# Kernel optimization log

Measured on AMD Instinct MI355X. Metric: run time of the kernel, lower is better.

## Reference

```python
import jax, jax.numpy as jnp
import numpy as np

D = 1024        # hidden_size = input_size = output_size
E = 8           # num_experts
K = 2           # top-k
TEMP = 1.0      # router temperature


def setup_inputs() -> dict:
    key = jax.random.key(0)
    ks = jax.random.split(key, 7)
    s = 0.02
    x = jax.random.normal(ks[0], (4, 2048, D), dtype=jnp.float32)
    w_router = jax.random.normal(ks[1], (D, E), dtype=jnp.float32) * s
    w1 = jax.random.normal(ks[2], (E, D, D), dtype=jnp.float32) * s
    b1 = jnp.zeros((E, D), dtype=jnp.float32)
    w2 = jax.random.normal(ks[3], (E, D, D), dtype=jnp.float32) * s
    b2 = jnp.zeros((E, D), dtype=jnp.float32)
    return {"x": x, "w_router": w_router, "w1": w1, "b1": b1, "w2": w2, "b2": b2}


def reference(x, w_router, w1, b1, w2, b2):
    B, S, _ = x.shape
    # Router: temperature-scaled logits, softmax, top-k
    logits = jnp.einsum('bsd,de->bse', x, w_router) / TEMP          # [B,S,E]
    probs = jax.nn.softmax(logits, axis=-1)
    top_k_probs, top_k_idx = jax.lax.top_k(probs, K)                # [B,S,K]
    xt = x.reshape(-1, D)                                           # [T,D]
    idx = top_k_idx.reshape(-1, K)                                  # [T,K]
    pk = top_k_probs.reshape(-1, K)                                 # [T,K]
    # Dense expert eval: every expert on every token (faithful to source)
    h = jax.nn.gelu(jnp.einsum('td,edh->eth', xt, w1) + b1[:, None, :])
    expert_out = jnp.einsum('eth,ehd->etd', h, w2) + b2[:, None, :]  # [E,T,D]
    expert_out = jnp.transpose(expert_out, (1, 0, 2))                # [T,E,D]
    # Gather selected experts and combine with routing probs
    sel = jnp.take_along_axis(expert_out, idx[:, :, None], axis=1)   # [T,K,D]
    combined = jnp.sum(sel * pk[:, :, None], axis=1)                 # [T,D]
    return combined.reshape(B, S, D), logits
```

## Files before the change

kernel.cpp:

```cpp
#include <hip/hip_runtime.h>
#include <hip/hip_bf16.h>

#define DH 1024
#define NE 8
#define NT 8192
#define NTK 16384
#define BM 128
#define BN 128
#define BK 64
#define KT (DH / BK)

typedef __bf16 bf16x8 __attribute__((ext_vector_type(8)));
typedef float f32x4 __attribute__((ext_vector_type(4)));
typedef unsigned short u16;
typedef u16 u16x8 __attribute__((ext_vector_type(8)));
typedef u16 u16x4 __attribute__((ext_vector_type(4)));

__device__ __forceinline__ u16 f2bf(float f) {
  union { float f; unsigned u; } v; v.f = f;
  return (u16)((v.u + 0x7fffu + ((v.u >> 16) & 1u)) >> 16);
}
__device__ __forceinline__ float bf2f(u16 h) {
  union { unsigned u; float f; } v; v.u = ((unsigned)h) << 16;
  return v.f;
}
__device__ __forceinline__ float gelu_tanh(float v) {
  float y = 0.7978845608028654f * (v + 0.044715f * v * v * v);
  float t = 1.f - 2.f / (1.f + __expf(2.f * y));
  return 0.5f * v * (1.f + t);
}

__device__ __forceinline__ void gload_lds16(const u16* g, u16* l) {
  __builtin_amdgcn_global_load_lds(
      (const __attribute__((address_space(1))) void*)g,
      (__attribute__((address_space(3))) void*)l, 16, 0, 0);
}

__global__ __launch_bounds__(256) void prep_transpose(
    const float* __restrict__ w1, const float* __restrict__ w2,
    u16* __restrict__ w1t, u16* __restrict__ w2t) {
  __shared__ float tile[64][65];
  int z = blockIdx.z;
  const float* src = (z < NE) ? (w1 + (size_t)z * DH * DH) : (w2 + (size_t)(z - NE) * DH * DH);
  u16* dst = (z < NE) ? (w1t + (size_t)z * DH * DH) : (w2t + (size_t)(z - NE) * DH * DH);
  int d0 = blockIdx.y * 64, n0 = blockIdx.x * 64;
  int tid = threadIdx.x;
  int c = tid & 63, r = tid >> 6;
#pragma unroll
  for (int it = 0; it < 16; ++it) {
    int rr = r + it * 4;
    tile[rr][c] = src[(size_t)(d0 + rr) * DH + n0 + c];
  }
  __syncthreads();
#pragma unroll
  for (int it = 0; it < 16; ++it) {
    int rr = r + it * 4;
    dst[(size_t)(n0 + rr) * DH + d0 + c] = f2bf(tile[c][rr]);
  }
}

__global__ __launch_bounds__(256) void router_kernel(
    const float* __restrict__ x, const float* __restrict__ wr,
    float* __restrict__ logits_out, int* __restrict__ tkidx,
    float* __restrict__ tkp, int* __restrict__ counts,
    u16* __restrict__ xb) {
  __shared__ float wsh[NE][DH + 8];
  __shared__ int hist[NE];
  int tid = threadIdx.x;
  for (int i = tid; i < DH * NE; i += 256) {
    int d = i >> 3, e = i & 7;
    wsh[e][d] = wr[i];
  }
  if (tid < NE) hist[tid] = 0;
  __syncthreads();

  int lane = tid & 63;
  int wv = tid >> 6;
  int t0 = blockIdx.x * 32 + wv * 8;
#pragma unroll 1
  for (int i = 0; i < 8; ++i) {
    int t = t0 + i;
    const float4* xp = (const float4*)(x + (size_t)t * DH);
    u16* xbrow = xb + (size_t)t * DH;
    float a[8] = {0.f, 0.f, 0.f, 0.f, 0.f, 0.f, 0.f, 0.f};
#pragma unroll
    for (int it = 0; it < 4; ++it) {
      float4 xv = xp[it * 64 + lane];
      int d0 = (it * 64 + lane) * 4;
      u16x4 c4;
      c4[0] = f2bf(xv.x); c4[1] = f2bf(xv.y); c4[2] = f2bf(xv.z); c4[3] = f2bf(xv.w);
      *(u16x4*)(xbrow + d0) = c4;
#pragma unroll
      for (int e = 0; e < 8; ++e) {
        float4 w4 = *(const float4*)&wsh[e][d0];
        a[e] += xv.x * w4.x + xv.y * w4.y + xv.z * w4.z + xv.w * w4.w;
      }
    }
#pragma unroll
    for (int off = 32; off; off >>= 1) {
#pragma unroll
      for (int e = 0; e < 8; ++e) a[e] += __shfl_xor(a[e], off, 64);
    }
    if (lane < 8) logits_out[(size_t)t * NE + lane] = a[lane];
    if (lane == 0) {
      float m1 = a[0]; int i1 = 0;
#pragma unroll
      for (int e = 1; e < 8; ++e) if (a[e] > m1) { m1 = a[e]; i1 = e; }
      float m2 = -3.4e38f; int i2 = 0;
#pragma unroll
      for (int e = 0; e < 8; ++e) if (e != i1 && a[e] > m2) { m2 = a[e]; i2 = e; }
      float den = 0.f;
#pragma unroll
      for (int e = 0; e < 8; ++e) den += expf(a[e] - m1);
      tkidx[2 * t] = i1; tkidx[2 * t + 1] = i2;
      tkp[2 * t] = 1.0f / den;
      tkp[2 * t + 1] = expf(m2 - m1) / den;
      atomicAdd(&hist[i1], 1);
      atomicAdd(&hist[i2], 1);
    }
  }
  __syncthreads();
  if (tid < NE) atomicAdd(&counts[tid], hist[tid]);
}

__global__ void offsets_kernel(const int* __restrict__ counts,
                               int* __restrict__ offs, int* __restrict__ cur,
                               int* __restrict__ tmap) {
  if (threadIdx.x == 0) {
    int s = 0;
    for (int e = 0; e < NE; ++e) { offs[e] = s; s += counts[e]; cur[e] = 0; }
    offs[NE] = s;
    int t = 0;
    for (int e = 0; e < NE; ++e)
      for (int m0 = 0; m0 < counts[e]; m0 += BM) {
        tmap[1 + 2 * t] = e; tmap[2 + 2 * t] = m0; ++t;
      }
    tmap[0] = t;
  }
}

__global__ __launch_bounds__(1024) void scatter_kernel(
    const int* __restrict__ tkidx, const float* __restrict__ tkp,
    const int* __restrict__ offs, int* __restrict__ cur,
    int* __restrict__ rows, int* __restrict__ posof, float* __restrict__ pp) {
  __shared__ int h[NE];
  __shared__ int base[NE];
  int tid = threadIdx.x;
  int gid = blockIdx.x * 1024 + tid;
  if (tid < NE) h[tid] = 0;
  __syncthreads();
  int e = tkidx[gid];
  int myrank = atomicAdd(&h[e], 1);
  __syncthreads();
  if (tid < NE) base[tid] = atomicAdd(&cur[tid], h[tid]);
  __syncthreads();
  int pos = offs[e] + base[e] + myrank;
  rows[pos] = gid >> 1;
  posof[gid] = pos;
  pp[pos] = tkp[gid];
}

template <int GELU>
__global__ __launch_bounds__(256, 2) void gemm_kernel(
    const u16* __restrict__ A, const u16* __restrict__ W,
    const float* __restrict__ bias, const int* __restrict__ counts,
    const int* __restrict__ offs, const int* __restrict__ rows,
    const int* __restrict__ tmap, u16* __restrict__ outb) {
  int ty = blockIdx.y;
  if (ty >= tmap[0]) return;
  int e = tmap[1 + 2 * ty];
  int m0 = tmap[2 + 2 * ty];
  int cnt = counts[e];
  int seg = offs[e];
  int n0 = blockIdx.x * BN;

  __shared__ __attribute__((aligned(16))) u16 lds[2][(BM + BN) * BK];

  int tid = threadIdx.x;
  int lane = tid & 63;
  int wv = tid >> 6;

  int srow = tid >> 3;
  int schunk = ((tid & 7) ^ ((tid >> 3) & 7)) * 8;
  const u16* aSrc[4];
  const u16* bSrc[4];
#pragma unroll
  for (int i = 0; i < 4; ++i) {
    int gi = m0 + i * 32 + srow;
    int cl = gi < cnt ? gi : cnt - 1;
    int arow = GELU ? rows[seg + cl] : (seg + cl);
    aSrc[i] = A + (size_t)arow * DH + schunk;
    bSrc[i] = W + (size_t)e * DH * DH + (size_t)(n0 + i * 32 + srow) * DH + schunk;
  }

  auto stage = [&](int d, int k0) {
    u16* base = &lds[d][0];
#pragma unroll
    for (int i = 0; i < 4; ++i) {
      gload_lds16(aSrc[i] + k0, base + (i * 32 + wv * 8) * BK);
      gload_lds16(bSrc[i] + k0, base + BM * BK + (i * 32 + wv * 8) * BK);
    }
  };

  int lr = lane & 15;
  int quad = lane >> 4;
  int sx = lr & 7;
  int k0off = (quad ^ sx) * 8;
  int k1off = ((4 + quad) ^ sx) * 8;
  int wrr = (wv >> 1) * 64, wcc = (wv & 1) * 64;

  f32x4 acc[4][4] = {};

  auto compute = [&](int d) {
    const u16* Ab = &lds[d][0];
    const u16* Bb = &lds[d][BM * BK];
    bf16x8 bfr[2][4];
#pragma unroll
    for (int n = 0; n < 4; ++n) {
      const u16* br = Bb + (size_t)(wcc + n * 16 + lr) * BK;
      bfr[0][n] = *(const bf16x8*)(br + k0off);
      bfr[1][n] = *(const bf16x8*)(br + k1off);
    }
    __builtin_amdgcn_s_setprio(1);
#pragma unroll
    for (int m = 0; m < 4; ++m) {
      const u16* ar = Ab + (size_t)(wrr + m * 16 + lr) * BK;
      bf16x8 a0 = *(const bf16x8*)(ar + k0off);
      bf16x8 a1 = *(const bf16x8*)(ar + k1off);
#pragma unroll
      for (int n = 0; n < 4; ++n) {
        acc[m][n] = __builtin_amdgcn_mfma_f32_16x16x32_bf16(a0, bfr[0][n], acc[m][n], 0, 0, 0);
        acc[m][n] = __builtin_amdgcn_mfma_f32_16x16x32_bf16(a1, bfr[1][n], acc[m][n], 0, 0, 0);
      }
    }
    __builtin_amdgcn_s_setprio(0);
  };

  stage(0, 0);
  stage(1, BK);
#pragma unroll 1
  for (int t = 0; t < KT - 2; ++t) {
    asm volatile("s_waitcnt vmcnt(8)" ::: "memory");
    __builtin_amdgcn_s_barrier();
    asm volatile("" ::: "memory");
    compute(t & 1);
    asm volatile("" ::: "memory");
    __builtin_amdgcn_s_barrier();
    stage(t & 1, (t + 2) * BK);
  }
  asm volatile("s_waitcnt vmcnt(8)" ::: "memory");
  __builtin_amdgcn_s_barrier();
  asm volatile("" ::: "memory");
  compute((KT - 2) & 1);
  asm volatile("s_waitcnt vmcnt(0)" ::: "memory");
  __builtin_amdgcn_s_barrier();
  asm volatile("" ::: "memory");
  compute((KT - 1) & 1);

  int r4 = quad * 4;
  const float* be = bias + (size_t)e * DH;
#pragma unroll
  for (int m = 0; m < 4; ++m) {
#pragma unroll
    for (int n = 0; n < 4; ++n) {
      int col = n0 + wcc + n * 16 + lr;
      float bvv = be[col];
#pragma unroll
      for (int j = 0; j < 4; ++j) {
        int gr = m0 + wrr + m * 16 + r4 + j;
        if (gr < cnt) {
          float v = acc[m][n][j] + bvv;
          if (GELU) v = gelu_tanh(v);
          outb[(size_t)(seg + gr) * DH + col] = f2bf(v);
        }
      }
    }
  }
}

__global__ __launch_bounds__(256) void combine_kernel(
    const u16* __restrict__ eo, const float* __restrict__ tkp,
    const int* __restrict__ posof, float* __restrict__ out) {
  int gid = blockIdx.x * 256 + threadIdx.x;
  int t = gid >> 8;
  int n = (gid & 255) * 4;
  float p0 = tkp[2 * t], p1 = tkp[2 * t + 1];
  int q0 = posof[2 * t], q1 = posof[2 * t + 1];
  u16x4 a = *(const u16x4*)(eo + (size_t)q0 * DH + n);
  u16x4 b = *(const u16x4*)(eo + (size_t)q1 * DH + n);
  float4 o;
  o.x = p0 * bf2f(a[0]) + p1 * bf2f(b[0]);
  o.y = p0 * bf2f(a[1]) + p1 * bf2f(b[1]);
  o.z = p0 * bf2f(a[2]) + p1 * bf2f(b[2]);
  o.w = p0 * bf2f(a[3]) + p1 * bf2f(b[3]);
  *(float4*)(out + (size_t)t * DH + n) = o;
}

extern "C" void kernel_launch(void* const* d_in, const int* in_sizes, int n_in,
                              void* d_out, int out_size, void* d_ws, size_t ws_size,
                              hipStream_t stream) {
  const float* x = (const float*)d_in[0];
  const float* w_router = (const float*)d_in[1];
  const float* w1 = (const float*)d_in[2];
  const float* b1 = (const float*)d_in[3];
  const float* w2 = (const float*)d_in[4];
  const float* b2 = (const float*)d_in[5];
  float* out = (float*)d_out;
  float* logits = out + (size_t)NT * DH;

  char* ws = (char*)d_ws;
  size_t off = 0;
  auto alloc = [&](size_t bytes) -> void* {
    void* p = ws + off;
    off = (off + bytes + 255) & ~(size_t)255;
    return p;
  };
  int* ctrl = (int*)alloc(256);
  int* counts = ctrl;
  int* cur = ctrl + 8;
  int* offs = ctrl + 16;
  int* tmap = (int*)alloc(2048);
  int* tkidx = (int*)alloc((size_t)NTK * 4);
  float* tkp = (float*)alloc((size_t)NTK * 4);
  int* rows = (int*)alloc((size_t)NTK * 4);
  int* posof = (int*)alloc((size_t)NTK * 4);
  float* pp = (float*)alloc((size_t)NTK * 4);
  u16* w1t = (u16*)alloc((size_t)NE * DH * DH * 2);
  u16* w2t = (u16*)alloc((size_t)NE * DH * DH * 2);
  u16* hbuf = (u16*)alloc((size_t)NTK * DH * 2);
  u16* eo = (u16*)alloc((size_t)NTK * DH * 2);
  u16* xb = eo;

  hipMemsetAsync(ctrl, 0, 256, stream);

  prep_transpose<<<dim3(16, 16, 16), 256, 0, stream>>>(w1, w2, w1t, w2t);
  router_kernel<<<NT / 32, 256, 0, stream>>>(x, w_router, logits, tkidx, tkp, counts, xb);
  offsets_kernel<<<1, 64, 0, stream>>>(counts, offs, cur, tmap);
  scatter_kernel<<<NTK / 1024, 1024, 0, stream>>>(tkidx, tkp, offs, cur, rows, posof, pp);
  gemm_kernel<1><<<dim3(8, 136, 1), 256, 0, stream>>>(xb, w1t, b1, counts, offs, rows, tmap, hbuf);
  gemm_kernel<0><<<dim3(8, 136, 1), 256, 0, stream>>>(hbuf, w2t, b2, counts, offs, rows, tmap, eo);
  combine_kernel<<<NT, 256, 0, stream>>>(eo, tkp, posof, out);
}
```

Before: 220.5 us.

## Vectorize weight transpose, swizzle GEMM tile order, restructure K-loop pipeline

The weight prep transpose now reads float4 and writes 4-wide bf16 vectors instead of scalars. The GEMM remaps block indices so tiles sharing an expert and N column are scheduled together, which should improve L2 reuse. The K-loop changes from a two-stage prefetch with partial waits to issuing the next stage before compute and then waiting for all loads, with one barrier per iteration. All A and B fragments are loaded before the MFMA burst. The new loop waits on vmcnt(0) every iteration, so less latency can hide behind compute, and holding all fragments at once raises register pressure.

```diff
diff --git a/kernel.cpp b/kernel.cpp
--- a/kernel.cpp
+++ b/kernel.cpp
@@ -45,17 +45,23 @@
   u16* dst = (z < NE) ? (w1t + (size_t)z * DH * DH) : (w2t + (size_t)(z - NE) * DH * DH);
   int d0 = blockIdx.y * 64, n0 = blockIdx.x * 64;
   int tid = threadIdx.x;
-  int c = tid & 63, r = tid >> 6;
-#pragma unroll
-  for (int it = 0; it < 16; ++it) {
-    int rr = r + it * 4;
-    tile[rr][c] = src[(size_t)(d0 + rr) * DH + n0 + c];
-  }
-  __syncthreads();
-#pragma unroll
-  for (int it = 0; it < 16; ++it) {
-    int rr = r + it * 4;
-    dst[(size_t)(n0 + rr) * DH + d0 + c] = f2bf(tile[c][rr]);
+  int r16 = tid >> 4;
+  int c4 = (tid & 15) * 4;
+#pragma unroll
+  for (int it = 0; it < 4; ++it) {
+    int rr = it * 16 + r16;
+    float4 v = *(const float4*)&src[(size_t)(d0 + rr) * DH + n0 + c4];
+    tile[rr][c4] = v.x; tile[rr][c4 + 1] = v.y;
+    tile[rr][c4 + 2] = v.z; tile[rr][c4 + 3] = v.w;
+  }
+  __syncthreads();
+#pragma unroll
+  for (int it = 0; it < 4; ++it) {
+    int n = it * 16 + r16;
+    u16x4 o;
+    o[0] = f2bf(tile[c4][n]);     o[1] = f2bf(tile[c4 + 1][n]);
+    o[2] = f2bf(tile[c4 + 2][n]); o[3] = f2bf(tile[c4 + 3][n]);
+    *(u16x4*)&dst[(size_t)(n0 + n) * DH + d0 + c4] = o;
   }
 }
 
@@ -166,13 +172,15 @@
     const float* __restrict__ bias, const int* __restrict__ counts,
     const int* __restrict__ offs, const int* __restrict__ rows,
     const int* __restrict__ tmap, u16* __restrict__ outb) {
-  int ty = blockIdx.y;
+  int orig = blockIdx.y * 8 + blockIdx.x;
+  int tile = (orig & 7) * 136 + (orig >> 3);
+  int ty = tile >> 3, tx = tile & 7;
   if (ty >= tmap[0]) return;
   int e = tmap[1 + 2 * ty];
   int m0 = tmap[2 + 2 * ty];
   int cnt = counts[e];
   int seg = offs[e];
-  int n0 = blockIdx.x * BN;
+  int n0 = tx * BN;
 
   __shared__ __attribute__((aligned(16))) u16 lds[2][(BM + BN) * BK];
 
@@ -180,17 +188,18 @@
   int lane = tid & 63;
   int wv = tid >> 6;
 
-  int srow = tid >> 3;
-  int schunk = ((tid & 7) ^ ((tid >> 3) & 7)) * 8;
+  int lrow = lane >> 3;
+  int schunk = ((lane & 7) ^ (lrow & 7)) * 8;
   const u16* aSrc[4];
   const u16* bSrc[4];
 #pragma unroll
   for (int i = 0; i < 4; ++i) {
-    int gi = m0 + i * 32 + srow;
+    int gi = m0 + i * 32 + wv * 8 + lrow;
     int cl = gi < cnt ? gi : cnt - 1;
     int arow = GELU ? rows[seg + cl] : (seg + cl);
     aSrc[i] = A + (size_t)arow * DH + schunk;
-    bSrc[i] = W + (size_t)e * DH * DH + (size_t)(n0 + i * 32 + srow) * DH + schunk;
+    int gn = n0 + i * 32 + wv * 8 + lrow;
+    bSrc[i] = W + (size_t)e * DH * DH + (size_t)gn * DH + schunk;
   }
 
   auto stage = [&](int d, int k0) {
@@ -214,48 +223,40 @@
   auto compute = [&](int d) {
     const u16* Ab = &lds[d][0];
     const u16* Bb = &lds[d][BM * BK];
-    bf16x8 bfr[2][4];
+    bf16x8 a0[4], a1[4], b0[4], b1[4];
 #pragma unroll
     for (int n = 0; n < 4; ++n) {
       const u16* br = Bb + (size_t)(wcc + n * 16 + lr) * BK;
-      bfr[0][n] = *(const bf16x8*)(br + k0off);
-      bfr[1][n] = *(const bf16x8*)(br + k1off);
-    }
-    __builtin_amdgcn_s_setprio(1);
+      b0[n] = *(const bf16x8*)(br + k0off);
+      b1[n] = *(const bf16x8*)(br + k1off);
+    }
 #pragma unroll
     for (int m = 0; m < 4; ++m) {
       const u16* ar = Ab + (size_t)(wrr + m * 16 + lr) * BK;
-      bf16x8 a0 = *(const bf16x8*)(ar + k0off);
-      bf16x8 a1 = *(const bf16x8*)(ar + k1off);
+      a0[m] = *(const bf16x8*)(ar + k0off);
+      a1[m] = *(const bf16x8*)(ar + k1off);
+    }
+    __builtin_amdgcn_s_setprio(1);
+#pragma unroll
+    for (int m = 0; m < 4; ++m)
 #pragma unroll
       for (int n = 0; n < 4; ++n) {
-        acc[m][n] = __builtin_amdgcn_mfma_f32_16x16x32_bf16(a0, bfr[0][n], acc[m][n], 0, 0, 0);
-        acc[m][n] = __builtin_amdgcn_mfma_f32_16x16x32_bf16(a1, bfr[1][n], acc[m][n], 0, 0, 0);
+        acc[m][n] = __builtin_amdgcn_mfma_f32_16x16x32_bf16(a0[m], b0[n], acc[m][n], 0, 0, 0);
+        acc[m][n] = __builtin_amdgcn_mfma_f32_16x16x32_bf16(a1[m], b1[n], acc[m][n], 0, 0, 0);
       }
-    }
     __builtin_amdgcn_s_setprio(0);
   };
 
   stage(0, 0);
-  stage(1, BK);
-#pragma unroll 1
-  for (int t = 0; t < KT - 2; ++t) {
-    asm volatile("s_waitcnt vmcnt(8)" ::: "memory");
-    __builtin_amdgcn_s_barrier();
-    asm volatile("" ::: "memory");
-    compute(t & 1);
-    asm volatile("" ::: "memory");
-    __builtin_amdgcn_s_barrier();
-    stage(t & 1, (t + 2) * BK);
-  }
-  asm volatile("s_waitcnt vmcnt(8)" ::: "memory");
-  __builtin_amdgcn_s_barrier();
-  asm volatile("" ::: "memory");
-  compute((KT - 2) & 1);
   asm volatile("s_waitcnt vmcnt(0)" ::: "memory");
   __builtin_amdgcn_s_barrier();
-  asm volatile("" ::: "memory");
-  compute((KT - 1) & 1);
+#pragma unroll 1
+  for (int t = 0; t < KT; ++t) {
+    if (t + 1 < KT) stage((t + 1) & 1, (t + 1) * BK);
+    compute(t & 1);
+    asm volatile("s_waitcnt vmcnt(0)" ::: "memory");
+    __builtin_amdgcn_s_barrier();
+  }
 
   int r4 = quad * 4;
   const float* be = bias + (size_t)e * DH;
```

New measurement: 209.3 us. 1.05x faster.
